# Performance work log

Measured on AMD Instinct MI355X. Metric: run time of the kernel, lower is better.

The kernel has to match this reference:

```python
import jax, jax.numpy as jnp
import numpy as np

N_SUM, N_MAX, M, HID, OUT, E, L = 2048, 64, 16, 128, 64, 16384, 4


def setup_inputs() -> dict:
    key = jax.random.key(0)
    ks = jax.random.split(key, 8)
    inp = {}
    inp["W"] = jax.random.normal(ks[0], (N_SUM, N_MAX, M), jnp.float32)
    inp["mask"] = jnp.ones((N_SUM, N_MAX), jnp.float32)
    inp["src"] = jax.random.randint(ks[1], (E,), 0, N_SUM)
    inp["dst"] = jax.random.randint(ks[2], (E,), 0, N_SUM)
    # GIN parameters: per-layer eps, MLP (Linear -> BN -> ReLU -> Linear)
    inp["eps"] = jax.random.normal(ks[3], (L,), jnp.float32)
    inp["W1_first"] = jax.random.normal(ks[4], (M, HID), jnp.float32) / np.sqrt(M).astype(np.float32)
    inp["b1_first"] = jnp.zeros((HID,), jnp.float32)
    inp["W1_rest"] = jax.random.normal(ks[5], (L - 1, HID, HID), jnp.float32) / np.sqrt(HID).astype(np.float32)
    inp["b1_rest"] = jnp.zeros((L - 1, HID), jnp.float32)
    inp["bn_gamma"] = jnp.ones((L, HID), jnp.float32)
    inp["bn_beta"] = jnp.zeros((L, HID), jnp.float32)
    inp["W2_mid"] = jax.random.normal(ks[6], (L - 1, HID, HID), jnp.float32) / np.sqrt(HID).astype(np.float32)
    inp["b2_mid"] = jnp.zeros((L - 1, HID), jnp.float32)
    inp["W2_last"] = jax.random.normal(ks[7], (HID, OUT), jnp.float32) / np.sqrt(HID).astype(np.float32)
    inp["b2_last"] = jnp.zeros((OUT,), jnp.float32)
    return inp


def _batchnorm(Hf, gamma, beta):
    # training-mode BatchNorm1d over flattened leading dims (biased variance)
    mu = Hf.mean(axis=0)
    var = Hf.var(axis=0)
    return (Hf - mu) * jax.lax.rsqrt(var + 1e-5) * gamma + beta


def _gin_layer(X, src, dst, eps, W1, b1, gamma, beta, W2, b2):
    # scatter-add message passing: gather sources, segment-sum into targets
    S = jax.ops.segment_sum(X[src], dst, num_segments=X.shape[0])  # [N_sum, n_max, D]
    Z = (1.0 + eps) * X + S
    H = Z @ W1 + b1                     # [N_sum, n_max, HID]
    shp = H.shape
    H = _batchnorm(H.reshape(-1, shp[-1]), gamma, beta)
    H = jax.nn.relu(H).reshape(shp)
    return H @ W2 + b2


def reference(W, mask, src, dst, eps, W1_first, b1_first, W1_rest, b1_rest,
              bn_gamma, bn_beta, W2_mid, b2_mid, W2_last, b2_last):
    X = W
    for l in range(L):
        W1 = W1_first if l == 0 else W1_rest[l - 1]
        b1 = b1_first if l == 0 else b1_rest[l - 1]
        W2 = W2_mid[l] if l < L - 1 else W2_last
        b2 = b2_mid[l] if l < L - 1 else b2_last
        X = _gin_layer(X, src, dst, eps[l], W1, b1, bn_gamma[l], bn_beta[l], W2, b2)
    # masked sum over the padded node axis -> positional encodings [N_sum, OUT]
    PE = (X * mask[:, :, None]).sum(axis=1)
    return PE
```

## Files before the change

### kernel.cpp

```cpp
#include <hip/hip_runtime.h>

#define N_SUM 2048
#define HIDD 128
#define NEDGE 16384
#define ROWS (N_SUM * 64)

typedef short short8 __attribute__((ext_vector_type(8)));
typedef float floatx4 __attribute__((ext_vector_type(4)));
typedef unsigned int uint4n __attribute__((ext_vector_type(4)));
typedef unsigned short ushort_t;

__device__ __forceinline__ ushort_t f2bf(float f) {
    unsigned u = __builtin_bit_cast(unsigned, f);
    u += 0x7fffu + ((u >> 16) & 1u);
    return (ushort_t)(u >> 16);
}
__device__ __forceinline__ float bf2f(ushort_t h) {
    return __builtin_bit_cast(float, (unsigned)h << 16);
}
__device__ __forceinline__ void unpack8(uint4 v, float* f) {
    f[0] = bf2f(v.x & 0xffff); f[1] = bf2f(v.x >> 16);
    f[2] = bf2f(v.y & 0xffff); f[3] = bf2f(v.y >> 16);
    f[4] = bf2f(v.z & 0xffff); f[5] = bf2f(v.z >> 16);
    f[6] = bf2f(v.w & 0xffff); f[7] = bf2f(v.w >> 16);
}
__device__ __forceinline__ uint4 pack8(const float* f) {
    uint4 v;
    v.x = f2bf(f[0]) | ((unsigned)f2bf(f[1]) << 16);
    v.y = f2bf(f[2]) | ((unsigned)f2bf(f[3]) << 16);
    v.z = f2bf(f[4]) | ((unsigned)f2bf(f[5]) << 16);
    v.w = f2bf(f[6]) | ((unsigned)f2bf(f[7]) << 16);
    return v;
}
__device__ __forceinline__ void nt_store16(const void* src, void* dst) {
    __builtin_nontemporal_store(*(const uint4n*)src, (uint4n*)dst);
}

__global__ __launch_bounds__(256) void zero_ints(int* p, int n) {
    int i = blockIdx.x * 256 + threadIdx.x;
    if (i < n) p[i] = 0;
}

__global__ __launch_bounds__(256) void count_deg(const int* __restrict__ dst, int* __restrict__ deg) {
    int e = blockIdx.x * 256 + threadIdx.x;
    if (e < NEDGE) atomicAdd(&deg[dst[e]], 1);
}

__global__ __launch_bounds__(256) void scan_deg(const int* __restrict__ deg, int* __restrict__ row_ptr) {
    __shared__ int csum[256];
    int t = threadIdx.x;
    int loc[8];
    int s = 0;
#pragma unroll
    for (int q = 0; q < 8; q++) { loc[q] = s; s += deg[t * 8 + q]; }
    csum[t] = s;
    __syncthreads();
    for (int off = 1; off < 256; off <<= 1) {
        int v = (t >= off) ? csum[t - off] : 0;
        __syncthreads();
        csum[t] += v;
        __syncthreads();
    }
    int base = (t == 0) ? 0 : csum[t - 1];
#pragma unroll
    for (int q = 0; q < 8; q++) row_ptr[t * 8 + q] = base + loc[q];
    if (t == 255) row_ptr[2048] = csum[255];
}

__global__ __launch_bounds__(256) void fill_csr(const int* __restrict__ src, const int* __restrict__ dst,
                                                const int* __restrict__ row_ptr, int* __restrict__ cursor,
                                                int* __restrict__ col) {
    int e = blockIdx.x * 256 + threadIdx.x;
    if (e < NEDGE) {
        int d = dst[e];
        int pos = atomicAdd(&cursor[d], 1);
        col[row_ptr[d] + pos] = src[e];
    }
}

__global__ __launch_bounds__(256) void prep_small(const float* __restrict__ W1f, const float* __restrict__ W2l,
                                                  const float* __restrict__ b2m, const float* __restrict__ W1r,
                                                  ushort_t* __restrict__ w1t0, ushort_t* __restrict__ w2lt,
                                                  float* __restrict__ bvec) {
    int idx = blockIdx.x * 256 + threadIdx.x;
    if (idx < 4096) {
        int nn = idx >> 5, k = idx & 31;
        w1t0[idx] = f2bf(k < 16 ? W1f[k * 128 + nn] : 0.f);
    } else if (idx < 4096 + 8192) {
        int r = idx - 4096;
        int nn = r >> 7, k = r & 127;
        w2lt[r] = f2bf(W2l[k * 64 + nn]);
    } else if (idx < 4096 + 8192 + 384) {
        int r = idx - 12288;
        int lm = r >> 7, c = r & 127;
        float s = 0.f;
        for (int o = 0; o < 128; o++) s += b2m[lm * 128 + o] * W1r[(size_t)lm * 16384 + o * 128 + c];
        bvec[r] = s;
    }
}

__global__ __launch_bounds__(256) void prep_w21(const float* __restrict__ W2m, const float* __restrict__ W1r,
                                                ushort_t* __restrict__ w21t) {
    int idx = blockIdx.x * 256 + threadIdx.x;
    int lm = idx >> 14, r = idx & 16383, i = r >> 7, c = r & 127;
    const float* w2row = W2m + (size_t)lm * 16384 + i * 128;
    const float* w1col = W1r + (size_t)lm * 16384 + c;
    float s = 0.f;
#pragma unroll 8
    for (int o = 0; o < 128; o++) s += w2row[o] * w1col[o * 128];
    w21t[(size_t)lm * 16384 + c * 128 + i] = f2bf(s);
}


__global__ __launch_bounds__(256, 4) void gin_mm1_l0(const float* __restrict__ Xf, const ushort_t* __restrict__ W1t,
                                                     const float* __restrict__ b1, const float* __restrict__ eps,
                                                     const int* __restrict__ rp, const int* __restrict__ colv,
                                                     ushort_t* __restrict__ H, float* __restrict__ partial) {
    __shared__ ushort_t Zs[64 * 128];
    int tid = threadIdx.x, n = blockIdx.x;
    float ev = 1.0f + eps[0];
    int e0 = rp[n], e1 = rp[n + 1], deg = e1 - e0;
    const float4* X = (const float4*)Xf;

    float4 sA, sB;
    sA = X[(size_t)n * 256 + tid];
    if (deg > 0) sB = X[(size_t)colv[e0] * 256 + tid];
    float4 a;
    a.x = sA.x * ev; a.y = sA.y * ev; a.z = sA.z * ev; a.w = sA.w * ev;
    int i = 1;
    for (; i + 1 < deg; i += 2) {
        sA = X[(size_t)colv[e0 + i] * 256 + tid];
        a.x += sB.x; a.y += sB.y; a.z += sB.z; a.w += sB.w;
        sB = X[(size_t)colv[e0 + i + 1] * 256 + tid];
        a.x += sA.x; a.y += sA.y; a.z += sA.z; a.w += sA.w;
    }
    if (deg > 0) {
        if (i < deg) {
            sA = X[(size_t)colv[e0 + i] * 256 + tid];
            a.x += sB.x; a.y += sB.y; a.z += sB.z; a.w += sB.w;
            a.x += sA.x; a.y += sA.y; a.z += sA.z; a.w += sA.w;
        } else {
            a.x += sB.x; a.y += sB.y; a.z += sB.z; a.w += sB.w;
        }
    }

    {
        int m = tid >> 2, k0 = (tid & 3) * 4;
        int addr = ((k0 >> 3) * 64 + m) * 8 + (k0 & 7);
        uint2 pv;
        pv.x = f2bf(a.x) | ((unsigned)f2bf(a.y) << 16);
        pv.y = f2bf(a.z) | ((unsigned)f2bf(a.w) << 16);
        *(uint2*)&Zs[addr] = pv;
        *(uint2*)&Zs[1024 + tid * 4] = make_uint2(0u, 0u);
    }
    __syncthreads();

    int w = tid >> 6, lane = tid & 63, lg = lane >> 4, ln = lane & 15;
    floatx4 C[4][2];
#pragma unroll
    for (int mt = 0; mt < 4; mt++) { C[mt][0] = {0.f, 0.f, 0.f, 0.f}; C[mt][1] = {0.f, 0.f, 0.f, 0.f}; }

    {
        short8 B0 = *(const short8*)&W1t[(w * 32 + ln) * 32 + lg * 8];
        short8 B1 = *(const short8*)&W1t[(w * 32 + 16 + ln) * 32 + lg * 8];
#pragma unroll
        for (int mt = 0; mt < 4; mt++) {
            short8 A = *(const short8*)&Zs[(lg * 64 + mt * 16 + ln) * 8];
            C[mt][0] = __builtin_amdgcn_mfma_f32_16x16x32_bf16(A, B0, C[mt][0], 0, 0, 0);
            C[mt][1] = __builtin_amdgcn_mfma_f32_16x16x32_bf16(A, B1, C[mt][1], 0, 0, 0);
        }
    }

    float bsum[2], bsq[2];
    float bv[2] = {b1[w * 32 + ln], b1[w * 32 + 16 + ln]};
#pragma unroll
    for (int nt = 0; nt < 2; nt++) {
        float s = 0.f, s2 = 0.f;
#pragma unroll
        for (int mt = 0; mt < 4; mt++)
#pragma unroll
            for (int r = 0; r < 4; r++) {
                float v = C[mt][nt][r] + bv[nt];
                C[mt][nt][r] = v;
                s += v; s2 += v * v;
            }
        bsum[nt] = s; bsq[nt] = s2;
    }
#pragma unroll
    for (int nt = 0; nt < 2; nt++) {
        bsum[nt] += __shfl_xor(bsum[nt], 16, 64);
        bsum[nt] += __shfl_xor(bsum[nt], 32, 64);
        bsq[nt] += __shfl_xor(bsq[nt], 16, 64);
        bsq[nt] += __shfl_xor(bsq[nt], 32, 64);
    }
    if (lg == 0) {
        int c0 = w * 32 + ln;
        __builtin_nontemporal_store(bsum[0], &partial[(size_t)n * 256 + c0]);
        __builtin_nontemporal_store(bsum[1], &partial[(size_t)n * 256 + c0 + 16]);
        __builtin_nontemporal_store(bsq[0], &partial[(size_t)n * 256 + 128 + c0]);
        __builtin_nontemporal_store(bsq[1], &partial[(size_t)n * 256 + 128 + c0 + 16]);
    }
    __syncthreads();
#pragma unroll
    for (int nt = 0; nt < 2; nt++) {
        int colc = w * 32 + nt * 16 + ln;
        int base = (colc >> 3) * 512 + (colc & 7);
#pragma unroll
        for (int mt = 0; mt < 4; mt++)
#pragma unroll
            for (int r = 0; r < 4; r++) {
                int row = mt * 16 + lg * 4 + r;
                Zs[base + row * 8] = f2bf(C[mt][nt][r]);
            }
    }
    __syncthreads();
#pragma unroll
    for (int q = 0; q < 4; q++)
        nt_store16(&((const uint4*)Zs)[q * 256 + tid], &((uint4*)&H[(size_t)n * 8192])[q * 256 + tid]);
}

__global__ __launch_bounds__(512, 4) void gin_mm1_fused(const ushort_t* __restrict__ Hin,
                                                        const ushort_t* __restrict__ W21t,
                                                        const float* __restrict__ b1, const float* __restrict__ bvec,
                                                        const float* __restrict__ scshp, const float* __restrict__ epsp,
                                                        const int* __restrict__ rp, const int* __restrict__ colv,
                                                        ushort_t* __restrict__ Hout, float* __restrict__ partial) {
    __shared__ ushort_t Zs[64 * 128];
    __shared__ float scs_lds[256];
    int tid = threadIdx.x, n = blockIdx.x;
    if (tid < 256) scs_lds[tid] = scshp[tid];
    __syncthreads();

    unsigned scp[2][8];
#pragma unroll
    for (int q = 0; q < 2; q++) {
        int cb = ((q * 512 + tid) >> 6) * 8;
#pragma unroll
        for (int j = 0; j < 8; j++)
            scp[q][j] = ((unsigned)f2bf(scs_lds[cb + j])) | ((unsigned)f2bf(scs_lds[128 + cb + j]) << 16);
    }

    float ev = 1.0f + epsp[0];
    int e0 = rp[n], e1 = rp[n + 1], deg = e1 - e0;
    const uint4* X = (const uint4*)Hin;
    float acc[2][8];
    uint4 bufA[2], bufB[2];

    {
        const uint4* p = X + (size_t)n * 1024;
#pragma unroll
        for (int q = 0; q < 2; q++) bufA[q] = p[q * 512 + tid];
    }
    if (deg > 0) {
        const uint4* p = X + (size_t)colv[e0] * 1024;
#pragma unroll
        for (int q = 0; q < 2; q++) bufB[q] = p[q * 512 + tid];
    }

#pragma unroll
    for (int q = 0; q < 2; q++) {
        float f[8]; unpack8(bufA[q], f);
#pragma unroll
        for (int j = 0; j < 8; j++) {
            float sc = __builtin_bit_cast(float, scp[q][j] << 16);
            float sh = __builtin_bit_cast(float, scp[q][j] & 0xffff0000u);
            acc[q][j] = ev * fmaxf(fmaf(f[j], sc, sh), 0.f);
        }
    }

    auto loadslab = [&](uint4* buf, int node) {
        const uint4* p = X + (size_t)node * 1024;
#pragma unroll
        for (int q = 0; q < 2; q++) buf[q] = p[q * 512 + tid];
    };
    auto addslab = [&](const uint4* buf) {
#pragma unroll
        for (int q = 0; q < 2; q++) {
            float f[8]; unpack8(buf[q], f);
#pragma unroll
            for (int j = 0; j < 8; j++) {
                float sc = __builtin_bit_cast(float, scp[q][j] << 16);
                float sh = __builtin_bit_cast(float, scp[q][j] & 0xffff0000u);
                acc[q][j] += fmaxf(fmaf(f[j], sc, sh), 0.f);
            }
        }
    };

    int i = 1;
    for (; i + 1 < deg; i += 2) {
        loadslab(bufA, colv[e0 + i]);
        addslab(bufB);
        loadslab(bufB, colv[e0 + i + 1]);
        addslab(bufA);
    }
    if (deg > 0) {
        if (i < deg) {
            loadslab(bufA, colv[e0 + i]);
            addslab(bufB);
            addslab(bufA);
        } else {
            addslab(bufB);
        }
    }

#pragma unroll
    for (int q = 0; q < 2; q++) ((uint4*)Zs)[q * 512 + tid] = pack8(acc[q]);
    __syncthreads();

    int w = tid >> 6, lane = tid & 63, lg = lane >> 4, ln = lane & 15;
    floatx4 C[4];
#pragma unroll
    for (int mt = 0; mt < 4; mt++) C[mt] = {0.f, 0.f, 0.f, 0.f};

    for (int kb = 0; kb < 4; kb++) {
        short8 B = *(const short8*)&W21t[(w * 16 + ln) * 128 + kb * 32 + lg * 8];
#pragma unroll
        for (int mt = 0; mt < 4; mt++) {
            short8 A = *(const short8*)&Zs[((kb * 4 + lg) * 64 + mt * 16 + ln) * 8];
            C[mt] = __builtin_amdgcn_mfma_f32_16x16x32_bf16(A, B, C[mt], 0, 0, 0);
        }
    }

    float fac = ev + (float)deg;
    int c0 = w * 16 + ln;
    float bv = b1[c0] + fac * bvec[c0];
    float s = 0.f, s2 = 0.f;
#pragma unroll
    for (int mt = 0; mt < 4; mt++)
#pragma unroll
        for (int r = 0; r < 4; r++) {
            float v = C[mt][r] + bv;
            C[mt][r] = v;
            s += v; s2 += v * v;
        }
    s += __shfl_xor(s, 16, 64);
    s += __shfl_xor(s, 32, 64);
    s2 += __shfl_xor(s2, 16, 64);
    s2 += __shfl_xor(s2, 32, 64);
    if (lg == 0) {
        __builtin_nontemporal_store(s, &partial[(size_t)n * 256 + c0]);
        __builtin_nontemporal_store(s2, &partial[(size_t)n * 256 + 128 + c0]);
    }

    __syncthreads();
    {
        int base = (c0 >> 3) * 512 + (c0 & 7);
#pragma unroll
        for (int mt = 0; mt < 4; mt++)
#pragma unroll
            for (int r = 0; r < 4; r++) {
                int row = mt * 16 + lg * 4 + r;
                Zs[base + row * 8] = f2bf(C[mt][r]);
            }
    }
    __syncthreads();
#pragma unroll
    for (int q = 0; q < 2; q++)
        nt_store16(&((const uint4*)Zs)[q * 512 + tid], &((uint4*)&Hout[(size_t)n * 8192])[q * 512 + tid]);
}

__global__ __launch_bounds__(256) void bn_stats(const float* __restrict__ partial, const float* __restrict__ gamma,
                                                const float* __restrict__ beta, float* __restrict__ scsh_out) {
    __shared__ float rs[256], rs2[256];
    int c = blockIdx.x, t = threadIdx.x;
    float s = 0.f, s2 = 0.f;
    for (int b = t; b < 2048; b += 256) {
        s += partial[(size_t)b * 256 + c];
        s2 += partial[(size_t)b * 256 + HIDD + c];
    }
    rs[t] = s; rs2[t] = s2;
    __syncthreads();
    for (int off = 128; off > 0; off >>= 1) {
        if (t < off) { rs[t] += rs[t + off]; rs2[t] += rs2[t + off]; }
        __syncthreads();
    }
    if (t == 0) {
        float mean = rs[0] / (float)ROWS;
        float var = rs2[0] / (float)ROWS - mean * mean;
        float sc = gamma[c] * rsqrtf(var + 1e-5f);
        scsh_out[c] = sc;
        scsh_out[HIDD + c] = beta[c] - mean * sc;
    }
}

__global__ __launch_bounds__(256, 4) void gin_mm2_last(const ushort_t* __restrict__ H, const ushort_t* __restrict__ W2t,
                                                       const float* __restrict__ b2, const float* __restrict__ scsh,
                                                       const float* __restrict__ mask, float* __restrict__ out) {
    __shared__ ushort_t Hs[64 * 128];
    int tid = threadIdx.x, n = blockIdx.x;

#pragma unroll
    for (int q = 0; q < 4; q++) {
        int c = q * 256 + tid;
        uint4 v = ((const uint4*)&H[(size_t)n * 8192])[c];
        float f[8]; unpack8(v, f);
        int cb = (c >> 6) * 8;
#pragma unroll
        for (int j = 0; j < 8; j++) f[j] = fmaxf(fmaf(f[j], scsh[cb + j], scsh[128 + cb + j]), 0.f);
        ((uint4*)Hs)[c] = pack8(f);
    }
    __syncthreads();

    int w = tid >> 6, lane = tid & 63, lg = lane >> 4, ln = lane & 15;
    floatx4 C[4];
#pragma unroll
    for (int mt = 0; mt < 4; mt++) C[mt] = {0.f, 0.f, 0.f, 0.f};

    for (int kb = 0; kb < 4; kb++) {
        short8 B = *(const short8*)&W2t[(w * 16 + ln) * 128 + kb * 32 + lg * 8];
#pragma unroll
        for (int mt = 0; mt < 4; mt++) {
            short8 A = *(const short8*)&Hs[((kb * 4 + lg) * 64 + mt * 16 + ln) * 8];
            C[mt] = __builtin_amdgcn_mfma_f32_16x16x32_bf16(A, B, C[mt], 0, 0, 0);
        }
    }

    int colc = w * 16 + ln;
    float bb = b2[colc];
    float pe = 0.f;
#pragma unroll
    for (int mt = 0; mt < 4; mt++)
#pragma unroll
        for (int r = 0; r < 4; r++) {
            int row = mt * 16 + lg * 4 + r;
            pe += mask[n * 64 + row] * (C[mt][r] + bb);
        }
    pe += __shfl_xor(pe, 16, 64);
    pe += __shfl_xor(pe, 32, 64);
    if (lg == 0) out[(size_t)n * 64 + colc] = pe;
}

extern "C" void kernel_launch(void* const* d_in, const int* in_sizes, int n_in, void* d_out, int out_size,
                              void* d_ws, size_t ws_size, hipStream_t stream) {
    const float* W    = (const float*)d_in[0];
    const float* mask = (const float*)d_in[1];
    const int* src    = (const int*)d_in[2];
    const int* dst    = (const int*)d_in[3];
    const float* eps  = (const float*)d_in[4];
    const float* W1f  = (const float*)d_in[5];
    const float* b1f  = (const float*)d_in[6];
    const float* W1r  = (const float*)d_in[7];
    const float* b1r  = (const float*)d_in[8];
    const float* gam  = (const float*)d_in[9];
    const float* bet  = (const float*)d_in[10];
    const float* W2m  = (const float*)d_in[11];
    const float* b2m  = (const float*)d_in[12];
    const float* W2l  = (const float*)d_in[13];
    const float* b2l  = (const float*)d_in[14];
    float* out = (float*)d_out;

    ushort_t* Ha   = (ushort_t*)d_ws;
    ushort_t* Hb   = Ha + 16777216;
    ushort_t* w1t0 = Hb + 16777216;
    ushort_t* w2lt = w1t0 + 4096;
    ushort_t* w21t = w2lt + 8192;
    float* bvec    = (float*)(w21t + 49152);
    float* partial = bvec + 384;
    float* scshL   = partial + 524288;
    int* ideg      = (int*)(scshL + 1024);
    int* icur      = ideg + 2048;
    int* irp       = icur + 2048;
    int* icol      = irp + 2052;

    zero_ints<<<16, 256, 0, stream>>>(ideg, 4096);
    count_deg<<<NEDGE / 256, 256, 0, stream>>>(dst, ideg);
    scan_deg<<<1, 256, 0, stream>>>(ideg, irp);
    fill_csr<<<NEDGE / 256, 256, 0, stream>>>(src, dst, irp, icur, icol);
    prep_small<<<50, 256, 0, stream>>>(W1f, W2l, b2m, W1r, w1t0, w2lt, bvec);
    prep_w21<<<192, 256, 0, stream>>>(W2m, W1r, w21t);

    gin_mm1_l0<<<N_SUM, 256, 0, stream>>>(W, w1t0, b1f, eps, irp, icol, Ha, partial);
    bn_stats<<<HIDD, 256, 0, stream>>>(partial, gam, bet, scshL);
    gin_mm1_fused<<<N_SUM, 512, 0, stream>>>(Ha, w21t, b1r, bvec, scshL, eps + 1, irp, icol, Hb, partial);
    bn_stats<<<HIDD, 256, 0, stream>>>(partial, gam + 128, bet + 128, scshL + 256);
    gin_mm1_fused<<<N_SUM, 512, 0, stream>>>(Hb, w21t + 16384, b1r + 128, bvec + 128, scshL + 256, eps + 2,
                                             irp, icol, Ha, partial);
    bn_stats<<<HIDD, 256, 0, stream>>>(partial, gam + 256, bet + 256, scshL + 512);
    gin_mm1_fused<<<N_SUM, 512, 0, stream>>>(Ha, w21t + 32768, b1r + 256, bvec + 256, scshL + 512, eps + 3,
                                             irp, icol, Hb, partial);
    bn_stats<<<HIDD, 256, 0, stream>>>(partial, gam + 384, bet + 384, scshL + 768);
    gin_mm2_last<<<N_SUM, 256, 0, stream>>>(Hb, w2lt, b2l, scshL + 768, mask, out);
}
```

Before: 309.2 us.

## Replace BN partial buffers and stats kernels with atomic sums; deepen gather prefetch

Per-block BatchNorm partial sums are now accumulated with global float atomics into a small sums buffer. The separate bn_stats kernels are removed and each consumer recomputes scale and shift from the sums in its prologue, cutting four launches and the partial-buffer round trip. Neighbor gathers now keep up to three loads in flight with a 4-deep rotating buffer instead of 2-deep. The fused kernel also keeps BN scale and shift in fp32 packed float2 and uses packed FMA and max, where before they were rounded to bf16. Risks are atomic contention on 256 addresses from 2048 blocks and nondeterministic summation order.

```diff
diff --git a/kernel.cpp b/kernel.cpp
--- a/kernel.cpp
+++ b/kernel.cpp
@@ -7,6 +7,7 @@
 
 typedef short short8 __attribute__((ext_vector_type(8)));
 typedef float floatx4 __attribute__((ext_vector_type(4)));
+typedef float float2v __attribute__((ext_vector_type(2)));
 typedef unsigned int uint4n __attribute__((ext_vector_type(4)));
 typedef unsigned short ushort_t;
 
@@ -17,6 +18,12 @@
 }
 __device__ __forceinline__ float bf2f(ushort_t h) {
     return __builtin_bit_cast(float, (unsigned)h << 16);
+}
+__device__ __forceinline__ float2v bfpair(unsigned u) {
+    float2v r;
+    r.x = __builtin_bit_cast(float, u << 16);
+    r.y = __builtin_bit_cast(float, u & 0xffff0000u);
+    return r;
 }
 __device__ __forceinline__ void unpack8(uint4 v, float* f) {
     f[0] = bf2f(v.x & 0xffff); f[1] = bf2f(v.x >> 16);
@@ -115,34 +122,38 @@
 __global__ __launch_bounds__(256, 4) void gin_mm1_l0(const float* __restrict__ Xf, const ushort_t* __restrict__ W1t,
                                                      const float* __restrict__ b1, const float* __restrict__ eps,
                                                      const int* __restrict__ rp, const int* __restrict__ colv,
-                                                     ushort_t* __restrict__ H, float* __restrict__ partial) {
+                                                     ushort_t* __restrict__ H, float* __restrict__ sums) {
     __shared__ ushort_t Zs[64 * 128];
     int tid = threadIdx.x, n = blockIdx.x;
     float ev = 1.0f + eps[0];
     int e0 = rp[n], e1 = rp[n + 1], deg = e1 - e0;
     const float4* X = (const float4*)Xf;
 
-    float4 sA, sB;
-    sA = X[(size_t)n * 256 + tid];
-    if (deg > 0) sB = X[(size_t)colv[e0] * 256 + tid];
+    float4 r0, r1, r2, r3;
+    r0 = X[(size_t)n * 256 + tid];
+    if (deg > 0) r1 = X[(size_t)colv[e0] * 256 + tid];
+    if (deg > 1) r2 = X[(size_t)colv[e0 + 1] * 256 + tid];
+    if (deg > 2) r3 = X[(size_t)colv[e0 + 2] * 256 + tid];
     float4 a;
-    a.x = sA.x * ev; a.y = sA.y * ev; a.z = sA.z * ev; a.w = sA.w * ev;
-    int i = 1;
-    for (; i + 1 < deg; i += 2) {
-        sA = X[(size_t)colv[e0 + i] * 256 + tid];
-        a.x += sB.x; a.y += sB.y; a.z += sB.z; a.w += sB.w;
-        sB = X[(size_t)colv[e0 + i + 1] * 256 + tid];
-        a.x += sA.x; a.y += sA.y; a.z += sA.z; a.w += sA.w;
-    }
-    if (deg > 0) {
-        if (i < deg) {
-            sA = X[(size_t)colv[e0 + i] * 256 + tid];
-            a.x += sB.x; a.y += sB.y; a.z += sB.z; a.w += sB.w;
-            a.x += sA.x; a.y += sA.y; a.z += sA.z; a.w += sA.w;
-        } else {
-            a.x += sB.x; a.y += sB.y; a.z += sB.z; a.w += sB.w;
-        }
-    }
+    a.x = r0.x * ev; a.y = r0.y * ev; a.z = r0.z * ev; a.w = r0.w * ev;
+    auto addf4 = [&](const float4& v) {
+        a.x += v.x; a.y += v.y; a.z += v.z; a.w += v.w;
+    };
+    int e = 0;
+    for (; e + 4 <= deg; e += 4) {
+        if (e + 3 < deg) r0 = X[(size_t)colv[e0 + e + 3] * 256 + tid];
+        addf4(r1);
+        if (e + 4 < deg) r1 = X[(size_t)colv[e0 + e + 4] * 256 + tid];
+        addf4(r2);
+        if (e + 5 < deg) r2 = X[(size_t)colv[e0 + e + 5] * 256 + tid];
+        addf4(r3);
+        if (e + 6 < deg) r3 = X[(size_t)colv[e0 + e + 6] * 256 + tid];
+        addf4(r0);
+    }
+    int rem = deg - e;
+    if (rem > 0) addf4(r1);
+    if (rem > 1) addf4(r2);
+    if (rem > 2) addf4(r3);
 
     {
         int m = tid >> 2, k0 = (tid & 3) * 4;
@@ -195,10 +206,10 @@
     }
     if (lg == 0) {
         int c0 = w * 32 + ln;
-        __builtin_nontemporal_store(bsum[0], &partial[(size_t)n * 256 + c0]);
-        __builtin_nontemporal_store(bsum[1], &partial[(size_t)n * 256 + c0 + 16]);
-        __builtin_nontemporal_store(bsq[0], &partial[(size_t)n * 256 + 128 + c0]);
-        __builtin_nontemporal_store(bsq[1], &partial[(size_t)n * 256 + 128 + c0 + 16]);
+        atomicAdd(&sums[c0], bsum[0]);
+        atomicAdd(&sums[c0 + 16], bsum[1]);
+        atomicAdd(&sums[128 + c0], bsq[0]);
+        atomicAdd(&sums[128 + c0 + 16], bsq[1]);
     }
     __syncthreads();
 #pragma unroll
@@ -222,89 +233,98 @@
 __global__ __launch_bounds__(512, 4) void gin_mm1_fused(const ushort_t* __restrict__ Hin,
                                                         const ushort_t* __restrict__ W21t,
                                                         const float* __restrict__ b1, const float* __restrict__ bvec,
-                                                        const float* __restrict__ scshp, const float* __restrict__ epsp,
+                                                        const float* __restrict__ sums_prev,
+                                                        const float* __restrict__ gam_prev,
+                                                        const float* __restrict__ bet_prev,
+                                                        const float* __restrict__ epsp,
                                                         const int* __restrict__ rp, const int* __restrict__ colv,
-                                                        ushort_t* __restrict__ Hout, float* __restrict__ partial) {
+                                                        ushort_t* __restrict__ Hout, float* __restrict__ sums_cur) {
     __shared__ ushort_t Zs[64 * 128];
     __shared__ float scs_lds[256];
     int tid = threadIdx.x, n = blockIdx.x;
-    if (tid < 256) scs_lds[tid] = scshp[tid];
-    __syncthreads();
-
-    unsigned scp[2][8];
+    if (tid < 128) {
+        float mean = sums_prev[tid] * (1.f / (float)ROWS);
+        float var = sums_prev[128 + tid] * (1.f / (float)ROWS) - mean * mean;
+        float sc = gam_prev[tid] * rsqrtf(var + 1e-5f);
+        scs_lds[tid] = sc;
+        scs_lds[128 + tid] = bet_prev[tid] - mean * sc;
+    }
+    __syncthreads();
+
+    float2v sc2[2][4], sh2[2][4];
 #pragma unroll
     for (int q = 0; q < 2; q++) {
         int cb = ((q * 512 + tid) >> 6) * 8;
 #pragma unroll
-        for (int j = 0; j < 8; j++)
-            scp[q][j] = ((unsigned)f2bf(scs_lds[cb + j])) | ((unsigned)f2bf(scs_lds[128 + cb + j]) << 16);
+        for (int i = 0; i < 4; i++) {
+            sc2[q][i].x = scs_lds[cb + 2 * i];     sc2[q][i].y = scs_lds[cb + 2 * i + 1];
+            sh2[q][i].x = scs_lds[128 + cb + 2 * i]; sh2[q][i].y = scs_lds[128 + cb + 2 * i + 1];
+        }
     }
 
     float ev = 1.0f + epsp[0];
     int e0 = rp[n], e1 = rp[n + 1], deg = e1 - e0;
     const uint4* X = (const uint4*)Hin;
-    float acc[2][8];
-    uint4 bufA[2], bufB[2];
-
-    {
-        const uint4* p = X + (size_t)n * 1024;
-#pragma unroll
-        for (int q = 0; q < 2; q++) bufA[q] = p[q * 512 + tid];
-    }
-    if (deg > 0) {
-        const uint4* p = X + (size_t)colv[e0] * 1024;
-#pragma unroll
-        for (int q = 0; q < 2; q++) bufB[q] = p[q * 512 + tid];
-    }
-
+    const float2v zero2 = {0.f, 0.f};
+
+    uint4 r0[2], r1[2], r2[2], r3[2];
+    auto ld = [&](uint4* buf, int node) {
+        const uint4* p = X + (size_t)node * 1024;
+        buf[0] = p[tid];
+        buf[1] = p[512 + tid];
+    };
+    ld(r0, n);
+    if (deg > 0) ld(r1, colv[e0]);
+    if (deg > 1) ld(r2, colv[e0 + 1]);
+    if (deg > 2) ld(r3, colv[e0 + 2]);
+
+    float2v acc[2][4];
 #pragma unroll
     for (int q = 0; q < 2; q++) {
-        float f[8]; unpack8(bufA[q], f);
-#pragma unroll
-        for (int j = 0; j < 8; j++) {
-            float sc = __builtin_bit_cast(float, scp[q][j] << 16);
-            float sh = __builtin_bit_cast(float, scp[q][j] & 0xffff0000u);
-            acc[q][j] = ev * fmaxf(fmaf(f[j], sc, sh), 0.f);
-        }
-    }
-
-    auto loadslab = [&](uint4* buf, int node) {
-        const uint4* p = X + (size_t)node * 1024;
-#pragma unroll
-        for (int q = 0; q < 2; q++) buf[q] = p[q * 512 + tid];
+        unsigned u[4] = {r0[q].x, r0[q].y, r0[q].z, r0[q].w};
+#pragma unroll
+        for (int i = 0; i < 4; i++) {
+            float2v t = __builtin_elementwise_fma(bfpair(u[i]), sc2[q][i], sh2[q][i]);
+            acc[q][i] = __builtin_elementwise_max(t, zero2) * ev;
+        }
+    }
+    auto addp = [&](const uint4* buf) {
+#pragma unroll
+        for (int q = 0; q < 2; q++) {
+            unsigned u[4] = {buf[q].x, buf[q].y, buf[q].z, buf[q].w};
+#pragma unroll
+            for (int i = 0; i < 4; i++) {
+                float2v t = __builtin_elementwise_fma(bfpair(u[i]), sc2[q][i], sh2[q][i]);
+                acc[q][i] += __builtin_elementwise_max(t, zero2);
+            }
+        }
     };
-    auto addslab = [&](const uint4* buf) {
-#pragma unroll
-        for (int q = 0; q < 2; q++) {
-            float f[8]; unpack8(buf[q], f);
-#pragma unroll
-            for (int j = 0; j < 8; j++) {
-                float sc = __builtin_bit_cast(float, scp[q][j] << 16);
-                float sh = __builtin_bit_cast(float, scp[q][j] & 0xffff0000u);
-                acc[q][j] += fmaxf(fmaf(f[j], sc, sh), 0.f);
-            }
-        }
-    };
-
-    int i = 1;
-    for (; i + 1 < deg; i += 2) {
-        loadslab(bufA, colv[e0 + i]);
-        addslab(bufB);
-        loadslab(bufB, colv[e0 + i + 1]);
-        addslab(bufA);
-    }
-    if (deg > 0) {
-        if (i < deg) {
-            loadslab(bufA, colv[e0 + i]);
-            addslab(bufB);
-            addslab(bufA);
-        } else {
-            addslab(bufB);
-        }
-    }
-
-#pragma unroll
-    for (int q = 0; q < 2; q++) ((uint4*)Zs)[q * 512 + tid] = pack8(acc[q]);
+
+    int e = 0;
+    for (; e + 4 <= deg; e += 4) {
+        if (e + 3 < deg) ld(r0, colv[e0 + e + 3]);
+        addp(r1);
+        if (e + 4 < deg) ld(r1, colv[e0 + e + 4]);
+        addp(r2);
+        if (e + 5 < deg) ld(r2, colv[e0 + e + 5]);
+        addp(r3);
+        if (e + 6 < deg) ld(r3, colv[e0 + e + 6]);
+        addp(r0);
+    }
+    int rem = deg - e;
+    if (rem > 0) addp(r1);
+    if (rem > 1) addp(r2);
+    if (rem > 2) addp(r3);
+
+#pragma unroll
+    for (int q = 0; q < 2; q++) {
+        uint4 pv;
+        pv.x = f2bf(acc[q][0].x) | ((unsigned)f2bf(acc[q][0].y) << 16);
+        pv.y = f2bf(acc[q][1].x) | ((unsigned)f2bf(acc[q][1].y) << 16);
+        pv.z = f2bf(acc[q][2].x) | ((unsigned)f2bf(acc[q][2].y) << 16);
+        pv.w = f2bf(acc[q][3].x) | ((unsigned)f2bf(acc[q][3].y) << 16);
+        ((uint4*)Zs)[q * 512 + tid] = pv;
+    }
     __syncthreads();
 
     int w = tid >> 6, lane = tid & 63, lg = lane >> 4, ln = lane & 15;
@@ -338,8 +358,8 @@
     s2 += __shfl_xor(s2, 16, 64);
     s2 += __shfl_xor(s2, 32, 64);
     if (lg == 0) {
-        __builtin_nontemporal_store(s, &partial[(size_t)n * 256 + c0]);
-        __builtin_nontemporal_store(s2, &partial[(size_t)n * 256 + 128 + c0]);
+        atomicAdd(&sums_cur[c0], s);
+        atomicAdd(&sums_cur[128 + c0], s2);
     }
 
     __syncthreads();
@@ -359,35 +379,23 @@
         nt_store16(&((const uint4*)Zs)[q * 512 + tid], &((uint4*)&Hout[(size_t)n * 8192])[q * 512 + tid]);
 }
 
-__global__ __launch_bounds__(256) void bn_stats(const float* __restrict__ partial, const float* __restrict__ gamma,
-                                                const float* __restrict__ beta, float* __restrict__ scsh_out) {
-    __shared__ float rs[256], rs2[256];
-    int c = blockIdx.x, t = threadIdx.x;
-    float s = 0.f, s2 = 0.f;
-    for (int b = t; b < 2048; b += 256) {
-        s += partial[(size_t)b * 256 + c];
-        s2 += partial[(size_t)b * 256 + HIDD + c];
-    }
-    rs[t] = s; rs2[t] = s2;
-    __syncthreads();
-    for (int off = 128; off > 0; off >>= 1) {
-        if (t < off) { rs[t] += rs[t + off]; rs2[t] += rs2[t + off]; }
-        __syncthreads();
-    }
-    if (t == 0) {
-        float mean = rs[0] / (float)ROWS;
-        float var = rs2[0] / (float)ROWS - mean * mean;
-        float sc = gamma[c] * rsqrtf(var + 1e-5f);
-        scsh_out[c] = sc;
-        scsh_out[HIDD + c] = beta[c] - mean * sc;
-    }
-}
-
 __global__ __launch_bounds__(256, 4) void gin_mm2_last(const ushort_t* __restrict__ H, const ushort_t* __restrict__ W2t,
-                                                       const float* __restrict__ b2, const float* __restrict__ scsh,
+                                                       const float* __restrict__ b2,
+                                                       const float* __restrict__ sums_prev,
+                                                       const float* __restrict__ gam_prev,
+                                                       const float* __restrict__ bet_prev,
                                                        const float* __restrict__ mask, float* __restrict__ out) {
     __shared__ ushort_t Hs[64 * 128];
+    __shared__ float scs_lds[256];
     int tid = threadIdx.x, n = blockIdx.x;
+    if (tid < 128) {
+        float mean = sums_prev[tid] * (1.f / (float)ROWS);
+        float var = sums_prev[128 + tid] * (1.f / (float)ROWS) - mean * mean;
+        float sc = gam_prev[tid] * rsqrtf(var + 1e-5f);
+        scs_lds[tid] = sc;
+        scs_lds[128 + tid] = bet_prev[tid] - mean * sc;
+    }
+    __syncthreads();
 
 #pragma unroll
     for (int q = 0; q < 4; q++) {
@@ -396,7 +404,7 @@
         float f[8]; unpack8(v, f);
         int cb = (c >> 6) * 8;
 #pragma unroll
-        for (int j = 0; j < 8; j++) f[j] = fmaxf(fmaf(f[j], scsh[cb + j], scsh[128 + cb + j]), 0.f);
+        for (int j = 0; j < 8; j++) f[j] = fmaxf(fmaf(f[j], scs_lds[cb + j], scs_lds[128 + cb + j]), 0.f);
         ((uint4*)Hs)[c] = pack8(f);
     }
     __syncthreads();
@@ -455,29 +463,25 @@
     ushort_t* w2lt = w1t0 + 4096;
     ushort_t* w21t = w2lt + 8192;
     float* bvec    = (float*)(w21t + 49152);
-    float* partial = bvec + 384;
-    float* scshL   = partial + 524288;
-    int* ideg      = (int*)(scshL + 1024);
+    int* ideg      = (int*)(bvec + 384);
     int* icur      = ideg + 2048;
-    int* irp       = icur + 2048;
+    float* sums    = (float*)(icur + 2048);
+    int* irp       = (int*)(sums + 1024);
     int* icol      = irp + 2052;
 
-    zero_ints<<<16, 256, 0, stream>>>(ideg, 4096);
+    zero_ints<<<20, 256, 0, stream>>>(ideg, 5120);
     count_deg<<<NEDGE / 256, 256, 0, stream>>>(dst, ideg);
     scan_deg<<<1, 256, 0, stream>>>(ideg, irp);
     fill_csr<<<NEDGE / 256, 256, 0, stream>>>(src, dst, irp, icur, icol);
     prep_small<<<50, 256, 0, stream>>>(W1f, W2l, b2m, W1r, w1t0, w2lt, bvec);
     prep_w21<<<192, 256, 0, stream>>>(W2m, W1r, w21t);
 
-    gin_mm1_l0<<<N_SUM, 256, 0, stream>>>(W, w1t0, b1f, eps, irp, icol, Ha, partial);
-    bn_stats<<<HIDD, 256, 0, stream>>>(partial, gam, bet, scshL);
-    gin_mm1_fused<<<N_SUM, 512, 0, stream>>>(Ha, w21t, b1r, bvec, scshL, eps + 1, irp, icol, Hb, partial);
-    bn_stats<<<HIDD, 256, 0, stream>>>(partial, gam + 128, bet + 128, scshL + 256);
-    gin_mm1_fused<<<N_SUM, 512, 0, stream>>>(Hb, w21t + 16384, b1r + 128, bvec + 128, scshL + 256, eps + 2,
-                                             irp, icol, Ha, partial);
-    bn_stats<<<HIDD, 256, 0, stream>>>(partial, gam + 256, bet + 256, scshL + 512);
-    gin_mm1_fused<<<N_SUM, 512, 0, stream>>>(Ha, w21t + 32768, b1r + 256, bvec + 256, scshL + 512, eps + 3,
-                                             irp, icol, Hb, partial);
-    bn_stats<<<HIDD, 256, 0, stream>>>(partial, gam + 384, bet + 384, scshL + 768);
-    gin_mm2_last<<<N_SUM, 256, 0, stream>>>(Hb, w2lt, b2l, scshL + 768, mask, out);
-}
+    gin_mm1_l0<<<N_SUM, 256, 0, stream>>>(W, w1t0, b1f, eps, irp, icol, Ha, sums);
+    gin_mm1_fused<<<N_SUM, 512, 0, stream>>>(Ha, w21t, b1r, bvec, sums, gam, bet, eps + 1,
+                                             irp, icol, Hb, sums + 256);
+    gin_mm1_fused<<<N_SUM, 512, 0, stream>>>(Hb, w21t + 16384, b1r + 128, bvec + 128, sums + 256,
+                                             gam + 128, bet + 128, eps + 2, irp, icol, Ha, sums + 512);
+    gin_mm1_fused<<<N_SUM, 512, 0, stream>>>(Ha, w21t + 32768, b1r + 256, bvec + 256, sums + 512,
+                                             gam + 256, bet + 256, eps + 3, irp, icol, Hb, sums + 768);
+    gin_mm2_last<<<N_SUM, 256, 0, stream>>>(Hb, w2lt, b2l, sums + 768, gam + 384, bet + 384, mask, out);
+}
```

Result: slower. 376.3 us (+21.7%).
